# Optimization experiments

Measured on AMD Instinct MI355X. Metric: run time of the kernel, lower is better.

## Reference

```python
import jax, jax.numpy as jnp
import numpy as np

N_NODES = 100000
N_EDGES = 3200000
D = 256


def setup_inputs() -> dict:
    key = jax.random.key(0)
    ks = jax.random.split(key, 8)
    ego_embeddings = jax.random.normal(ks[0], (N_NODES, D), dtype=jnp.float32) * 0.1
    edge_vals = jax.random.uniform(ks[1], (N_EDGES,), dtype=jnp.float32) / 32.0  # ~normalized adjacency
    W1 = jax.random.normal(ks[2], (D, D), dtype=jnp.float32) * (1.0 / np.sqrt(D))
    b1 = jnp.zeros((D,), dtype=jnp.float32)
    W2 = jax.random.normal(ks[3], (D, D), dtype=jnp.float32) * (1.0 / np.sqrt(D))
    b2 = jnp.zeros((D,), dtype=jnp.float32)
    edge_rows = jax.random.randint(ks[4], (N_EDGES,), 0, N_NODES, dtype=jnp.int32)
    edge_cols = jax.random.randint(ks[5], (N_EDGES,), 0, N_NODES, dtype=jnp.int32)
    return {"ego_embeddings": ego_embeddings, "edge_vals": edge_vals,
            "W1": W1, "b1": b1, "W2": W2, "b2": b2,
            "edge_rows": edge_rows, "edge_cols": edge_cols}


def reference(ego_embeddings, edge_vals, W1, b1, W2, b2, edge_rows, edge_cols):
    # SpMM: side = A_in @ ego  (A_in in COO: rows, cols, vals)
    n = ego_embeddings.shape[0]
    gathered = ego_embeddings[edge_cols] * edge_vals[:, None]      # [E, D]
    side = jax.ops.segment_sum(gathered, edge_rows, num_segments=n)  # [N, D]
    # bi-interaction aggregator
    sum_emb = jax.nn.leaky_relu((ego_embeddings + side) @ W1.T + b1, negative_slope=0.01)
    bi_emb = jax.nn.leaky_relu((ego_embeddings * side) @ W2.T + b2, negative_slope=0.01)
    # dropout p=0.0 -> identity
    return sum_emb + bi_emb
```

## Files before the change

kernel.cpp:

```cpp
#include <hip/hip_runtime.h>
#include <hip/hip_fp16.h>
#include <stdint.h>

#define D 256
#define CHSH 13

typedef __attribute__((ext_vector_type(8))) short short8;
typedef __attribute__((ext_vector_type(4))) float floatx4;

__device__ __forceinline__ ushort f2bf(float f) {
    union { float f; uint32_t u; } v; v.f = f;
    uint32_t u = v.u;
    u += 0x7fffu + ((u >> 16) & 1u);
    return (ushort)(u >> 16);
}
__device__ __forceinline__ float bf2f(ushort h) {
    union { uint32_t u; float f; } v; v.u = ((uint32_t)h) << 16;
    return v.f;
}


__global__ void k_hist(const int* __restrict__ er, const int* __restrict__ ec,
                       const float* __restrict__ ev,
                       int* __restrict__ bp, uint64_t* __restrict__ aux,
                       int E, int NCH) {
    int e = blockIdx.x * 256 + threadIdx.x;
    if (e >= E) return;
    int row = er[e];
    int col = ec[e];
    int b = row * NCH + (col >> CHSH);
    atomicAdd(&bp[b], 1);
    ushort hb = __half_as_ushort(__float2half_rn(ev[e]));
    uint32_t payload = ((uint32_t)col << 15) | (uint32_t)hb;
    aux[e] = ((uint64_t)(uint32_t)b << 32) | payload;
}

__global__ void k_red(const int* __restrict__ bp, int* __restrict__ part, int nb) {
    __shared__ int s[256];
    int t = threadIdx.x;
    int base = blockIdx.x * 1024 + t * 4;
    int v = 0;
#pragma unroll
    for (int j = 0; j < 4; ++j) if (base + j < nb) v += bp[base + j];
    s[t] = v; __syncthreads();
    for (int off = 128; off; off >>= 1) {
        if (t < off) s[t] += s[t + off];
        __syncthreads();
    }
    if (t == 0) part[blockIdx.x] = s[0];
}

__global__ __launch_bounds__(1024) void k_scanpart(int* __restrict__ part, int np) {
    __shared__ int s[1024];
    int t = threadIdx.x;
    int p0 = (2 * t < np) ? part[2 * t] : 0;
    int p1 = (2 * t + 1 < np) ? part[2 * t + 1] : 0;
    int v = p0 + p1;
    s[t] = v; __syncthreads();
    for (int off = 1; off < 1024; off <<= 1) {
        int x = (t >= off) ? s[t - off] : 0;
        __syncthreads();
        s[t] += x;
        __syncthreads();
    }
    int excl = s[t] - v;
    if (2 * t < np) part[2 * t] = excl;
    if (2 * t + 1 < np) part[2 * t + 1] = excl + p0;
}

__global__ void k_scan3(int* __restrict__ bp, const int* __restrict__ part, int nb) {
    __shared__ int s[256];
    int t = threadIdx.x;
    int base = blockIdx.x * 1024 + t * 4;
    int d0 = 0, d1 = 0, d2 = 0, d3 = 0;
    if (base     < nb) d0 = bp[base];
    if (base + 1 < nb) d1 = bp[base + 1];
    if (base + 2 < nb) d2 = bp[base + 2];
    if (base + 3 < nb) d3 = bp[base + 3];
    int sum = d0 + d1 + d2 + d3;
    s[t] = sum; __syncthreads();
    for (int off = 1; off < 256; off <<= 1) {
        int x = (t >= off) ? s[t - off] : 0;
        __syncthreads();
        s[t] += x;
        __syncthreads();
    }
    int run = part[blockIdx.x] + s[t] - sum;
    if (base     < nb) bp[base]     = run; run += d0;
    if (base + 1 < nb) bp[base + 1] = run; run += d1;
    if (base + 2 < nb) bp[base + 2] = run; run += d2;
    if (base + 3 < nb) bp[base + 3] = run;
}

__global__ void k_scatter(const uint64_t* __restrict__ aux,
                          int* __restrict__ bp, uint32_t* __restrict__ csr,
                          int E, int BW) {
    int xcd = blockIdx.x & 7;
    int j = blockIdx.x >> 3;
    int e = j * 256 + threadIdx.x;
    if (e >= E) return;
    uint64_t a = aux[e];
    int b = (int)(a >> 32);
    int lo = xcd * BW;
    if (b < lo || b >= lo + BW) return;
    int p = atomicAdd(&bp[b], 1);
    csr[p] = (uint32_t)a;
}

__global__ void k_cvt(const float4* __restrict__ ego, ushort4* __restrict__ ego_bf,
                      const float4* __restrict__ W1, const float4* __restrict__ W2,
                      ushort4* __restrict__ W1b, ushort4* __restrict__ W2b, int n4) {
    int i = blockIdx.x * 256 + threadIdx.x;
    const float4* src;
    ushort4* dst;
    if (i < n4) { src = ego + i; dst = ego_bf + i; }
    else {
        int j = i - n4;
        if (j >= 32768) return;
        int k = j & 16383;
        src = ((j < 16384) ? W1 : W2) + k;
        dst = ((j < 16384) ? W1b : W2b) + k;
    }
    float4 f = *src;
    ushort4 u;
    u.x = f2bf(f.x); u.y = f2bf(f.y); u.z = f2bf(f.z); u.w = f2bf(f.w);
    *dst = u;
}

__global__ void k_spmm(const ushort* __restrict__ ego_bf, const int* __restrict__ bp,
                       const uint32_t* __restrict__ csr,
                       ushort* __restrict__ X1, ushort* __restrict__ X2, int n, int NCH) {
    int gtid = blockIdx.x * 256 + threadIdx.x;
    int node = gtid >> 6;
    int lane = gtid & 63;
    if (node >= n) return;
    int beg = (node == 0) ? 0 : bp[node * NCH - 1];
    int end = bp[(node + 1) * NCH - 1];
    int d0 = lane * 4;
    float a0 = 0.f, a1 = 0.f, a2 = 0.f, a3 = 0.f;
    int e = beg;
    for (; e + 16 <= end; e += 16) {
        uint32_t w[16];
#pragma unroll
        for (int j = 0; j < 16; ++j) w[j] = csr[e + j];
        ushort4 u[16];
#pragma unroll
        for (int j = 0; j < 16; ++j)
            u[j] = *(const ushort4*)(ego_bf + (size_t)(w[j] >> 15) * D + d0);
#pragma unroll
        for (int j = 0; j < 16; ++j) {
            float v = __half2float(__ushort_as_half((ushort)(w[j] & 0x7fff)));
            a0 += v * bf2f(u[j].x);
            a1 += v * bf2f(u[j].y);
            a2 += v * bf2f(u[j].z);
            a3 += v * bf2f(u[j].w);
        }
    }
    if (e < end) {
        uint32_t w[16];
#pragma unroll
        for (int j = 0; j < 16; ++j) w[j] = (e + j < end) ? csr[e + j] : 0u;
        ushort4 u[16];
#pragma unroll
        for (int j = 0; j < 16; ++j)
            u[j] = *(const ushort4*)(ego_bf + (size_t)(w[j] >> 15) * D + d0);
#pragma unroll
        for (int j = 0; j < 16; ++j) {
            float v = __half2float(__ushort_as_half((ushort)(w[j] & 0x7fff)));
            a0 += v * bf2f(u[j].x);
            a1 += v * bf2f(u[j].y);
            a2 += v * bf2f(u[j].z);
            a3 += v * bf2f(u[j].w);
        }
    }
    ushort4 eg = *(const ushort4*)(ego_bf + (size_t)node * D + d0);
    float e0 = bf2f(eg.x), e1 = bf2f(eg.y), e2 = bf2f(eg.z), e3 = bf2f(eg.w);
    ushort4 o1, o2;
    o1.x = f2bf(e0 + a0); o2.x = f2bf(e0 * a0);
    o1.y = f2bf(e1 + a1); o2.y = f2bf(e1 * a1);
    o1.z = f2bf(e2 + a2); o2.z = f2bf(e2 * a2);
    o1.w = f2bf(e3 + a3); o2.w = f2bf(e3 * a3);
    *(ushort4*)(X1 + (size_t)node * D + d0) = o1;
    *(ushort4*)(X2 + (size_t)node * D + d0) = o2;
}

__global__ __launch_bounds__(256) void k_gemm(
        const ushort* __restrict__ X1, const ushort* __restrict__ X2,
        const ushort* __restrict__ W1b, const ushort* __restrict__ W2b,
        const float* __restrict__ b1, const float* __restrict__ b2,
        float* __restrict__ out, int n) {
    int lane = threadIdx.x & 63;
    int w = threadIdx.x >> 6;
    int l16 = lane & 15, quad = lane >> 4;
    int row0 = blockIdx.x * 64;
    int colw = w * 64;

    floatx4 acc1[4][4], acc2[4][4];
#pragma unroll
    for (int i = 0; i < 4; ++i)
#pragma unroll
        for (int j = 0; j < 4; ++j) { acc1[i][j] = (floatx4)0.f; acc2[i][j] = (floatx4)0.f; }

    for (int kk = 0; kk < D; kk += 32) {
        short8 a[4], b[4];
#pragma unroll
        for (int mt = 0; mt < 4; ++mt)
            a[mt] = *(const short8*)(X1 + (size_t)(row0 + mt * 16 + l16) * D + kk + quad * 8);
#pragma unroll
        for (int nt = 0; nt < 4; ++nt)
            b[nt] = *(const short8*)(W1b + (size_t)(colw + nt * 16 + l16) * D + kk + quad * 8);
#pragma unroll
        for (int mt = 0; mt < 4; ++mt)
#pragma unroll
            for (int nt = 0; nt < 4; ++nt)
                acc1[mt][nt] = __builtin_amdgcn_mfma_f32_16x16x32_bf16(a[mt], b[nt], acc1[mt][nt], 0, 0, 0);
    }
    for (int kk = 0; kk < D; kk += 32) {
        short8 a[4], b[4];
#pragma unroll
        for (int mt = 0; mt < 4; ++mt)
            a[mt] = *(const short8*)(X2 + (size_t)(row0 + mt * 16 + l16) * D + kk + quad * 8);
#pragma unroll
        for (int nt = 0; nt < 4; ++nt)
            b[nt] = *(const short8*)(W2b + (size_t)(colw + nt * 16 + l16) * D + kk + quad * 8);
#pragma unroll
        for (int mt = 0; mt < 4; ++mt)
#pragma unroll
            for (int nt = 0; nt < 4; ++nt)
                acc2[mt][nt] = __builtin_amdgcn_mfma_f32_16x16x32_bf16(a[mt], b[nt], acc2[mt][nt], 0, 0, 0);
    }

#pragma unroll
    for (int nt = 0; nt < 4; ++nt) {
        int col = colw + nt * 16 + l16;
        float bb1 = b1[col], bb2 = b2[col];
#pragma unroll
        for (int mt = 0; mt < 4; ++mt) {
            int row = row0 + mt * 16 + quad * 4;
#pragma unroll
            for (int r = 0; r < 4; ++r) {
                if (row + r < n) {
                    float v1 = acc1[mt][nt][r] + bb1;
                    v1 = v1 > 0.f ? v1 : 0.01f * v1;
                    float v2 = acc2[mt][nt][r] + bb2;
                    v2 = v2 > 0.f ? v2 : 0.01f * v2;
                    out[(size_t)(row + r) * D + col] = v1 + v2;
                }
            }
        }
    }
}

extern "C" void kernel_launch(void* const* d_in, const int* in_sizes, int n_in,
                              void* d_out, int out_size, void* d_ws, size_t ws_size,
                              hipStream_t stream) {
    const float* ego   = (const float*)d_in[0];
    const float* evals = (const float*)d_in[1];
    const float* W1    = (const float*)d_in[2];
    const float* b1    = (const float*)d_in[3];
    const float* W2    = (const float*)d_in[4];
    const float* b2    = (const float*)d_in[5];
    const int* erows   = (const int*)d_in[6];
    const int* ecols   = (const int*)d_in[7];
    float* out = (float*)d_out;

    int n = in_sizes[0] / D;
    int E = in_sizes[1];
    int npad = (n + 63) & ~63;
    int NCH = (n + (1 << CHSH) - 1) >> CHSH;
    int nb = n * NCH;
    int np = (nb + 1023) / 1024;
    int BW = (nb + 7) / 8;

    char* p = (char*)d_ws;
    auto alloc = [&](size_t bytes) {
        char* q = p;
        p += (bytes + 511) & ~(size_t)511;
        return q;
    };
    ushort* ego_bf = (ushort*)alloc((size_t)n * D * 2);
    ushort* X1     = (ushort*)alloc((size_t)npad * D * 2);
    ushort* X2     = (ushort*)alloc((size_t)npad * D * 2);
    ushort* W1b    = (ushort*)alloc((size_t)D * D * 2);
    ushort* W2b    = (ushort*)alloc((size_t)D * D * 2);
    int* bp        = (int*)alloc((size_t)nb * 4);
    int* part      = (int*)alloc((size_t)np * 4);
    uint32_t* csr  = (uint32_t*)alloc((size_t)E * 4);

    uint64_t* aux = (uint64_t*)X1;

    hipMemsetAsync(bp, 0, (size_t)nb * 4, stream);
    int EB = (E + 255) / 256;
    k_hist<<<EB, 256, 0, stream>>>(erows, ecols, evals, bp, aux, E, NCH);
    k_red<<<np, 256, 0, stream>>>(bp, part, nb);
    k_scanpart<<<1, 1024, 0, stream>>>(part, np);
    k_scan3<<<np, 256, 0, stream>>>(bp, part, nb);
    k_scatter<<<8 * EB, 256, 0, stream>>>(aux, bp, csr, E, BW);

    int n4 = n * (D / 4);
    k_cvt<<<(n4 + 32768 + 255) / 256, 256, 0, stream>>>((const float4*)ego, (ushort4*)ego_bf,
                                                        (const float4*)W1, (const float4*)W2,
                                                        (ushort4*)W1b, (ushort4*)W2b, n4);

    k_spmm<<<(n * 64 + 255) / 256, 256, 0, stream>>>(ego_bf, bp, csr, X1, X2, n, NCH);

    k_gemm<<<npad / 64, 256, 0, stream>>>(X1, X2, W1b, W2b, b1, b2, out, n);
}
```

Baseline: 831.5 us.

## Pre-bucket edge records by XCD range in histogram to avoid 8x scatter rereads

The histogram kernel now reads four edges per thread with vector loads. It also partitions each edge record into one of eight per-XCD buckets, using shared-memory counters plus one global atomic per bucket per block. The scatter kernel then reads only its own bucket instead of reading the whole aux array eight times and filtering by range, which removes most of the redundant aux traffic. In exchange it adds shared atomics and a fixed per-bucket capacity (E/8+65536) that could overflow on skewed inputs, and the scatter grid stays oversized.

```diff
diff --git a/kernel.cpp b/kernel.cpp
--- a/kernel.cpp
+++ b/kernel.cpp
@@ -20,19 +20,66 @@
 }
 
 
-__global__ void k_hist(const int* __restrict__ er, const int* __restrict__ ec,
-                       const float* __restrict__ ev,
-                       int* __restrict__ bp, uint64_t* __restrict__ aux,
-                       int E, int NCH) {
-    int e = blockIdx.x * 256 + threadIdx.x;
-    if (e >= E) return;
-    int row = er[e];
-    int col = ec[e];
-    int b = row * NCH + (col >> CHSH);
-    atomicAdd(&bp[b], 1);
-    ushort hb = __half_as_ushort(__float2half_rn(ev[e]));
-    uint32_t payload = ((uint32_t)col << 15) | (uint32_t)hb;
-    aux[e] = ((uint64_t)(uint32_t)b << 32) | payload;
+__global__ void k_hist(const int4* __restrict__ er4, const int4* __restrict__ ec4,
+                       const float4* __restrict__ ev4,
+                       int* __restrict__ bp, uint64_t* __restrict__ aux8,
+                       int* __restrict__ cnt8,
+                       int E, int NCH, int BW, int cap8) {
+    __shared__ int lcnt[8];
+    __shared__ int lbase[8];
+    int t = threadIdx.x;
+    if (t < 8) lcnt[t] = 0;
+    __syncthreads();
+
+    int q = blockIdx.x * 256 + t;
+    int e0 = q * 4;
+    int w_[4], r_[4];
+    uint64_t rec[4];
+    bool ok[4];
+    if (e0 + 3 < E) {
+        int4 rr = er4[q];
+        int4 cc = ec4[q];
+        float4 vv = ev4[q];
+        int rows[4] = {rr.x, rr.y, rr.z, rr.w};
+        int cols[4] = {cc.x, cc.y, cc.z, cc.w};
+        float vals[4] = {vv.x, vv.y, vv.z, vv.w};
+#pragma unroll
+        for (int k = 0; k < 4; ++k) {
+            int b = rows[k] * NCH + (cols[k] >> CHSH);
+            ok[k] = true;
+            atomicAdd(&bp[b], 1);
+            ushort hb = __half_as_ushort(__float2half_rn(vals[k]));
+            rec[k] = ((uint64_t)(uint32_t)b << 32) |
+                     (((uint32_t)cols[k] << 15) | (uint32_t)hb);
+            w_[k] = b / BW;
+            r_[k] = atomicAdd(&lcnt[w_[k]], 1);
+        }
+    } else {
+#pragma unroll
+        for (int k = 0; k < 4; ++k) {
+            int e = e0 + k;
+            ok[k] = (e < E);
+            if (ok[k]) {
+                int row = ((const int*)er4)[e];
+                int col = ((const int*)ec4)[e];
+                float val = ((const float*)ev4)[e];
+                int b = row * NCH + (col >> CHSH);
+                atomicAdd(&bp[b], 1);
+                ushort hb = __half_as_ushort(__float2half_rn(val));
+                rec[k] = ((uint64_t)(uint32_t)b << 32) |
+                         (((uint32_t)col << 15) | (uint32_t)hb);
+                w_[k] = b / BW;
+                r_[k] = atomicAdd(&lcnt[w_[k]], 1);
+            }
+        }
+    }
+    __syncthreads();
+    if (t < 8) lbase[t] = atomicAdd(&cnt8[t], lcnt[t]);
+    __syncthreads();
+#pragma unroll
+    for (int k = 0; k < 4; ++k)
+        if (ok[k])
+            aux8[(size_t)w_[k] * cap8 + lbase[w_[k]] + r_[k]] = rec[k];
 }
 
 __global__ void k_red(const int* __restrict__ bp, int* __restrict__ part, int nb) {
@@ -92,17 +139,13 @@
     if (base + 3 < nb) bp[base + 3] = run;
 }
 
-__global__ void k_scatter(const uint64_t* __restrict__ aux,
-                          int* __restrict__ bp, uint32_t* __restrict__ csr,
-                          int E, int BW) {
-    int xcd = blockIdx.x & 7;
-    int j = blockIdx.x >> 3;
-    int e = j * 256 + threadIdx.x;
-    if (e >= E) return;
-    uint64_t a = aux[e];
+__global__ void k_scatter(const uint64_t* __restrict__ aux8, const int* __restrict__ cnt8,
+                          int* __restrict__ bp, uint32_t* __restrict__ csr, int cap8) {
+    int w = blockIdx.x & 7;
+    int j = (blockIdx.x >> 3) * 256 + threadIdx.x;
+    if (j >= cnt8[w]) return;
+    uint64_t a = aux8[(size_t)w * cap8 + j];
     int b = (int)(a >> 32);
-    int lo = xcd * BW;
-    if (b < lo || b >= lo + BW) return;
     int p = atomicAdd(&bp[b], 1);
     csr[p] = (uint32_t)a;
 }
@@ -271,6 +314,7 @@
     int nb = n * NCH;
     int np = (nb + 1023) / 1024;
     int BW = (nb + 7) / 8;
+    int cap8 = E / 8 + 65536;
 
     char* p = (char*)d_ws;
     auto alloc = [&](size_t bytes) {
@@ -285,17 +329,22 @@
     ushort* W2b    = (ushort*)alloc((size_t)D * D * 2);
     int* bp        = (int*)alloc((size_t)nb * 4);
     int* part      = (int*)alloc((size_t)np * 4);
+    int* cnt8      = (int*)alloc(8 * 4);
     uint32_t* csr  = (uint32_t*)alloc((size_t)E * 4);
 
-    uint64_t* aux = (uint64_t*)X1;
+    uint64_t* aux8 = (uint64_t*)X1;
 
     hipMemsetAsync(bp, 0, (size_t)nb * 4, stream);
+    hipMemsetAsync(cnt8, 0, 8 * 4, stream);
     int EB = (E + 255) / 256;
-    k_hist<<<EB, 256, 0, stream>>>(erows, ecols, evals, bp, aux, E, NCH);
+    int EB4 = (E + 1023) / 1024;
+    k_hist<<<EB4, 256, 0, stream>>>((const int4*)erows, (const int4*)ecols,
+                                    (const float4*)evals, bp, aux8, cnt8,
+                                    E, NCH, BW, cap8);
     k_red<<<np, 256, 0, stream>>>(bp, part, nb);
     k_scanpart<<<1, 1024, 0, stream>>>(part, np);
     k_scan3<<<np, 256, 0, stream>>>(bp, part, nb);
-    k_scatter<<<8 * EB, 256, 0, stream>>>(aux, bp, csr, E, BW);
+    k_scatter<<<8 * EB, 256, 0, stream>>>(aux8, cnt8, bp, csr, cap8);
 
     int n4 = n * (D / 4);
     k_cvt<<<(n4 + 32768 + 255) / 256, 256, 0, stream>>>((const float4*)ego, (ushort4*)ego_bf,
```

Measured after the change: 941.6 us. 13.2% more time.
